# Optimization experiments

Measured on AMD Instinct MI355X. Metric: run time of the kernel, lower is better.

The kernel has to match this reference:

```python
import jax, jax.numpy as jnp
import numpy as np

N = 32767      # 2**15 - 1 nodes: complete binary tree, parent(i) = (i-1)//2
IN = 512       # in_channels
H = 256        # hidden_dim
OUT = 1        # output_dim
DEPTH = 15     # number of topological levels (static)


def setup_inputs() -> dict:
    key = jax.random.key(0)
    ks = jax.random.split(key, 8)
    x = jax.random.normal(ks[0], (N, IN), dtype=jnp.float32)
    # complete binary tree edge list: edge_index[0]=child, edge_index[1]=parent
    src = jnp.arange(1, N, dtype=jnp.int32)
    dst = (src - 1) // 2
    edge_index = jnp.stack([src, dst])  # [2, N-1]
    s = 1.0 / np.sqrt(H)  # torch LSTMCell/Linear default uniform init scale
    W_ih = jax.random.uniform(ks[1], (4 * H, IN), minval=-s, maxval=s, dtype=jnp.float32)
    W_hh = jax.random.uniform(ks[2], (4 * H, H), minval=-s, maxval=s, dtype=jnp.float32)
    b_ih = jax.random.uniform(ks[3], (4 * H,), minval=-s, maxval=s, dtype=jnp.float32)
    b_hh = jax.random.uniform(ks[4], (4 * H,), minval=-s, maxval=s, dtype=jnp.float32)
    W_fc = jax.random.uniform(ks[5], (OUT, H), minval=-s, maxval=s, dtype=jnp.float32)
    b_fc = jax.random.uniform(ks[6], (OUT,), minval=-s, maxval=s, dtype=jnp.float32)
    return {"x": x, "edge_index": edge_index, "W_ih": W_ih, "W_hh": W_hh,
            "b_ih": b_ih, "b_hh": b_hh, "W_fc": W_fc, "b_fc": b_fc}


def reference(x, edge_index, W_ih, W_hh, b_ih, b_hh, W_fc, b_fc):
    src, dst = edge_index[0], edge_index[1]
    # children count per parent (matches torch children_count loop)
    cnt = jax.ops.segment_sum(jnp.ones_like(src, dtype=x.dtype), dst, num_segments=N)
    cnt = jnp.maximum(cnt, 1.0)[:, None]  # [N,1]; leaves get zero child state anyway
    h = jnp.zeros((N, H), dtype=x.dtype)
    c = jnp.zeros((N, H), dtype=x.dtype)
    # topological sweep: deepest level first (children processed before parents)
    for d in range(DEPTH - 1, -1, -1):
        lo = 2 ** d - 1
        hi = min(2 ** (d + 1) - 1, N)  # level d node index range (static)
        # mean of already-computed child h/c states, gathered via edge list
        mean_h = jax.ops.segment_sum(h[src], dst, num_segments=N)[lo:hi] / cnt[lo:hi]
        mean_c = jax.ops.segment_sum(c[src], dst, num_segments=N)[lo:hi] / cnt[lo:hi]
        # torch LSTMCell: gates in (i, f, g, o) order
        gates = x[lo:hi] @ W_ih.T + b_ih + mean_h @ W_hh.T + b_hh  # [n_level, 4H]
        i, f, g, o = jnp.split(gates, 4, axis=-1)
        i, f, o = jax.nn.sigmoid(i), jax.nn.sigmoid(f), jax.nn.sigmoid(o)
        g = jnp.tanh(g)
        c_new = f * mean_c + i * g
        h_new = o * jnp.tanh(c_new)
        h = h.at[lo:hi].set(h_new)
        c = c.at[lo:hi].set(c_new)
    pooled = jnp.mean(h, axis=0, keepdims=True)  # [1, H]
    out = pooled @ W_fc.T + b_fc                 # [1, 1]
    return out.squeeze(-1)                       # [1]
```

## Files before the change

### kernel.cpp

```cpp
#include <hip/hip_runtime.h>
#include <hip/hip_cooperative_groups.h>
#include <math.h>

namespace cg = cooperative_groups;


#define N_NODES 32767
#define N_LEAF0 16383
#define IN_C    512
#define H_C     256

typedef __bf16 bf16x8 __attribute__((ext_vector_type(8)));
typedef float  f32x4  __attribute__((ext_vector_type(4)));

__device__ __forceinline__ void gload_lds16(const void* g, void* l) {
    __builtin_amdgcn_global_load_lds(
        (const __attribute__((address_space(1))) unsigned int*)g,
        (__attribute__((address_space(3))) unsigned int*)l,
        16, 0, 0);
}

__device__ __forceinline__ float fast_rcp(float x) { return __builtin_amdgcn_rcpf(x); }
__device__ __forceinline__ float sigm(float x)     { return fast_rcp(1.f + __expf(-x)); }
__device__ __forceinline__ float tanh_fast(float x){ return 2.f * fast_rcp(1.f + __expf(-2.f * x)) - 1.f; }

__global__ __launch_bounds__(256)
void conv_bf16_kernel(const float* __restrict__ src, __bf16* __restrict__ dst, int n8)
{
    const int i = blockIdx.x * 256 + threadIdx.x;
    if (i < n8) {
        const float4* s4 = (const float4*)src;
        const float4 a = s4[2 * i];
        const float4 b = s4[2 * i + 1];
        bf16x8 o;
        o[0] = (__bf16)a.x; o[1] = (__bf16)a.y; o[2] = (__bf16)a.z; o[3] = (__bf16)a.w;
        o[4] = (__bf16)b.x; o[5] = (__bf16)b.y; o[6] = (__bf16)b.z; o[7] = (__bf16)b.w;
        *(bf16x8*)(dst + 8 * i) = o;
    }
}

__global__ __launch_bounds__(256)
void bulk_xw(const float* __restrict__ x,
             const __bf16* __restrict__ wih,
             const float* __restrict__ b_ih,
             const float* __restrict__ b_hh,
             __bf16* __restrict__ hb,
             float* __restrict__ c,
             __bf16* __restrict__ gx)
{
    __shared__ __bf16 As[128 * 64];
    __shared__ __bf16 Bs[128 * 64];

    const int t    = threadIdx.x;
    const int lane = t & 63;
    const int wv   = t >> 6;
    const int wm   = wv >> 1;
    const int wn   = wv & 1;
    const int quad = lane >> 4;
    const int l15  = lane & 15;

    const int i  = blockIdx.x;
    const int cb = (i >> 3) & 7;
    const int mt = (i & 7) | ((i >> 6) << 3);
    const int m0 = mt * 128;

    f32x4 acc[4][4];
#pragma unroll
    for (int mi = 0; mi < 4; ++mi)
#pragma unroll
        for (int ni = 0; ni < 4; ++ni) acc[mi][ni] = (f32x4)0.f;

    for (int k0 = 0; k0 < IN_C; k0 += 64) {
#pragma unroll
        for (int e = 0; e < 4; ++e) {
            const int ch = (wv * 4 + e) * 64 + lane;
            const int nl = ch >> 3;
            const int k8 = (ch & 7) ^ (nl & 7);
            const int q  = (nl >> 4) & 3;
            const int cc = (nl & 15) | ((nl >> 6) << 4);
            const int grow = q * H_C + cb * 32 + cc;
            gload_lds16(wih + (size_t)grow * IN_C + k0 + k8 * 8,
                        (char*)Bs + (wv * 4 + e) * 1024);
        }
        {
            const int row  = t >> 1;
            const int kh   = (t & 1) * 32;
            const int node = min(m0 + row, N_NODES - 1);
            const float4* xs = (const float4*)(x + (size_t)node * IN_C + k0 + kh);
#pragma unroll
            for (int j = 0; j < 4; ++j) {
                const float4 v0 = xs[2 * j], v1 = xs[2 * j + 1];
                bf16x8 o;
                o[0] = (__bf16)v0.x; o[1] = (__bf16)v0.y; o[2] = (__bf16)v0.z; o[3] = (__bf16)v0.w;
                o[4] = (__bf16)v1.x; o[5] = (__bf16)v1.y; o[6] = (__bf16)v1.z; o[7] = (__bf16)v1.w;
                const int cs = ((kh >> 3) + j) ^ (row & 7);
                *(bf16x8*)(As + row * 64 + cs * 8) = o;
            }
        }
        __syncthreads();
#pragma unroll
        for (int ks = 0; ks < 2; ++ks) {
            bf16x8 af[4], bfr[4];
#pragma unroll
            for (int mi = 0; mi < 4; ++mi) {
                const int row = wm * 64 + mi * 16 + l15;
                af[mi] = *(const bf16x8*)(As + row * 64 + (((ks * 4 + quad) ^ (row & 7)) << 3));
            }
#pragma unroll
            for (int ni = 0; ni < 4; ++ni) {
                const int row = wn * 64 + ni * 16 + l15;
                bfr[ni] = *(const bf16x8*)(Bs + row * 64 + (((ks * 4 + quad) ^ (row & 7)) << 3));
            }
#pragma unroll
            for (int mi = 0; mi < 4; ++mi)
#pragma unroll
                for (int ni = 0; ni < 4; ++ni)
                    acc[mi][ni] = __builtin_amdgcn_mfma_f32_16x16x32_bf16(
                        af[mi], bfr[ni], acc[mi][ni], 0, 0, 0);
        }
        __syncthreads();
    }

    const int CH = cb * 32 + wn * 16 + l15;
    float bs[4];
#pragma unroll
    for (int q = 0; q < 4; ++q) bs[q] = b_ih[q * H_C + CH] + b_hh[q * H_C + CH];

#pragma unroll
    for (int mi = 0; mi < 4; ++mi) {
#pragma unroll
        for (int r = 0; r < 4; ++r) {
            const int m = m0 + wm * 64 + mi * 16 + quad * 4 + r;
            if (m >= N_NODES) continue;
            if (m >= N_LEAF0) {
                const float gi = sigm(acc[mi][0][r] + bs[0]);
                const float gf = sigm(acc[mi][1][r] + bs[1]);  (void)gf;
                const float gg = tanh_fast(acc[mi][2][r] + bs[2]);
                const float go = sigm(acc[mi][3][r] + bs[3]);
                const float cn = gi * gg;
                const float hn = go * tanh_fast(cn);
                c[(size_t)m * H_C + CH] = cn;
                hb[(size_t)m * H_C + CH] = (__bf16)hn;
            } else {
#pragma unroll
                for (int q = 0; q < 4; ++q)
                    gx[(size_t)m * 1024 + q * H_C + CH] = (__bf16)acc[mi][q][r];
            }
        }
    }
}

__global__ __launch_bounds__(256)
void level_hw(const __bf16* __restrict__ whh,
              const float* __restrict__ b_ih,
              const float* __restrict__ b_hh,
              const __bf16* __restrict__ gx,
              __bf16* __restrict__ hb,
              float* __restrict__ c,
              int lo, int n)
{
    __shared__ __bf16 As[128 * 32];
    __shared__ __bf16 Bs[128 * 32];

    const int t    = threadIdx.x;
    const int lane = t & 63;
    const int wv   = t >> 6;
    const int wm   = wv >> 1;
    const int wn   = wv & 1;
    const int quad = lane >> 4;
    const int l15  = lane & 15;

    const int i = blockIdx.x;
    int cb, mt;
    if (gridDim.x >= 64) { cb = (i >> 3) & 7; mt = (i & 7) | ((i >> 6) << 3); }
    else                 { cb = i & 7;        mt = i >> 3; }
    const int m0 = mt * 128;

    f32x4 acc[4][4];
#pragma unroll
    for (int mi = 0; mi < 4; ++mi)
#pragma unroll
        for (int ni = 0; ni < 4; ++ni) acc[mi][ni] = (f32x4)0.f;

    for (int k0 = 0; k0 < H_C; k0 += 32) {
#pragma unroll
        for (int e = 0; e < 2; ++e) {
            const int chunk = wv * 2 + e;
            const int nl    = chunk * 16 + (lane >> 2);
            const int q     = (nl >> 4) & 3;
            const int cc    = (nl & 15) + ((nl >> 6) << 4);
            const int grow  = q * H_C + cb * 32 + cc;
            const void* g = (const char*)(whh + grow * H_C + k0) + (lane & 3) * 16;
            gload_lds16(g, (char*)Bs + chunk * 1024);
        }
        {
            const int row  = t >> 1;
            const int kh   = (t & 1) * 16;
            const int node = lo + m0 + row;
            const int k2   = k0 + kh;
            const bf16x8* hl = (const bf16x8*)(hb + (size_t)(2 * node + 1) * H_C + k2);
            const bf16x8* hr = (const bf16x8*)(hb + (size_t)(2 * node + 2) * H_C + k2);
            const bf16x8 a0 = hl[0], a1 = hl[1], b0 = hr[0], b1 = hr[1];
            bf16x8 o0, o1;
#pragma unroll
            for (int j = 0; j < 8; ++j) {
                o0[j] = (__bf16)(0.5f * ((float)a0[j] + (float)b0[j]));
                o1[j] = (__bf16)(0.5f * ((float)a1[j] + (float)b1[j]));
            }
            bf16x8* dst = (bf16x8*)(As + row * 32 + kh);
            dst[0] = o0;
            dst[1] = o1;
        }
        __syncthreads();
        bf16x8 af[4], bfr[4];
#pragma unroll
        for (int mi = 0; mi < 4; ++mi)
            af[mi] = *(const bf16x8*)(As + (wm * 64 + mi * 16 + l15) * 32 + quad * 8);
#pragma unroll
        for (int ni = 0; ni < 4; ++ni)
            bfr[ni] = *(const bf16x8*)(Bs + (wn * 64 + ni * 16 + l15) * 32 + quad * 8);
#pragma unroll
        for (int mi = 0; mi < 4; ++mi)
#pragma unroll
            for (int ni = 0; ni < 4; ++ni)
                acc[mi][ni] = __builtin_amdgcn_mfma_f32_16x16x32_bf16(
                    af[mi], bfr[ni], acc[mi][ni], 0, 0, 0);
        __syncthreads();
    }

    const int CH = cb * 32 + wn * 16 + l15;
    float bs[4];
#pragma unroll
    for (int q = 0; q < 4; ++q) bs[q] = b_ih[q * H_C + CH] + b_hh[q * H_C + CH];

#pragma unroll
    for (int mi = 0; mi < 4; ++mi) {
#pragma unroll
        for (int r = 0; r < 4; ++r) {
            const int m = m0 + wm * 64 + mi * 16 + quad * 4 + r;
            if (m < n) {
                const int node = lo + m;
                const float g0 = acc[mi][0][r] + (float)gx[(size_t)node * 1024 + 0 * H_C + CH] + bs[0];
                const float g1 = acc[mi][1][r] + (float)gx[(size_t)node * 1024 + 1 * H_C + CH] + bs[1];
                const float g2 = acc[mi][2][r] + (float)gx[(size_t)node * 1024 + 2 * H_C + CH] + bs[2];
                const float g3 = acc[mi][3][r] + (float)gx[(size_t)node * 1024 + 3 * H_C + CH] + bs[3];
                const float gi = sigm(g0);
                const float gf = sigm(g1);
                const float gg = tanh_fast(g2);
                const float go = sigm(g3);
                const float mc = 0.5f * (c[(size_t)(2 * node + 1) * H_C + CH] +
                                         c[(size_t)(2 * node + 2) * H_C + CH]);
                const float cn = gf * mc + gi * gg;
                const float hn = go * tanh_fast(cn);
                c[(size_t)node * H_C + CH] = cn;
                hb[(size_t)node * H_C + CH] = (__bf16)hn;
            }
        }
    }
}

__global__ __launch_bounds__(256, 1)
void tail_levels(const __bf16* __restrict__ whh,
                 const float* __restrict__ b_ih,
                 const float* __restrict__ b_hh,
                 const __bf16* __restrict__ gx,
                 __bf16* __restrict__ hb,
                 const float* __restrict__ c)
{
    __shared__ __bf16 Ws[128][264];
    __shared__ __align__(16) char UAG[64 * 264 * 2];
    __shared__ float cl[2][64][33];

    const int t    = threadIdx.x;
    const int cb   = blockIdx.x;
    const int lane = t & 63;
    const int wq   = t >> 6;
    const int quad = lane >> 4;
    const int l15  = lane & 15;

    auto As = (__bf16(*)[264])UAG;
    auto Gs = (float(*)[64][33])UAG;

    {
        const int row = t >> 1;
        const int k0  = (t & 1) * 128;
        const int q   = row >> 5, cc = row & 31;
        const __bf16* src = whh + (size_t)(q * H_C + cb * 32 + cc) * H_C + k0;
#pragma unroll
        for (int j = 0; j < 16; ++j)
            *(bf16x8*)(&Ws[row][k0 + 8 * j]) = *(const bf16x8*)(src + 8 * j);
    }
    const int ecc = t & 31;
    const int erg = t >> 5;
    const int CH  = cb * 32 + ecc;
    float bsq[4];
#pragma unroll
    for (int q = 0; q < 4; ++q) bsq[q] = b_ih[q * H_C + CH] + b_hh[q * H_C + CH];

    cg::grid_group grid = cg::this_grid();

    for (int d = 6; d >= 0; --d) {
        const int n  = 1 << d;
        const int lo = n - 1;
        const int pp = d & 1;
        __syncthreads();
        {
            const int row  = t >> 2;
            const int kb   = (t & 3) * 64;
            const int node = lo + row;
            const bf16x8* hl = (const bf16x8*)(hb + (size_t)(2 * node + 1) * H_C + kb);
            const bf16x8* hr = (const bf16x8*)(hb + (size_t)(2 * node + 2) * H_C + kb);
#pragma unroll
            for (int j = 0; j < 8; ++j) {
                const bf16x8 a = hl[j], b = hr[j];
                bf16x8 o;
#pragma unroll
                for (int e = 0; e < 8; ++e)
                    o[e] = (__bf16)(0.5f * ((float)a[e] + (float)b[e]));
                *(bf16x8*)(&As[row][kb + 8 * j]) = o;
            }
        }
        __syncthreads();
        f32x4 acc[4][2];
#pragma unroll
        for (int mi = 0; mi < 4; ++mi)
#pragma unroll
            for (int ni = 0; ni < 2; ++ni) acc[mi][ni] = (f32x4)0.f;
        for (int kk = 0; kk < 8; ++kk) {
#pragma unroll
            for (int mi = 0; mi < 4; ++mi) {
                const bf16x8 af = *(const bf16x8*)(&As[mi * 16 + l15][kk * 32 + quad * 8]);
#pragma unroll
                for (int ni = 0; ni < 2; ++ni) {
                    const bf16x8 bf_ = *(const bf16x8*)(&Ws[wq * 32 + ni * 16 + l15][kk * 32 + quad * 8]);
                    acc[mi][ni] = __builtin_amdgcn_mfma_f32_16x16x32_bf16(af, bf_, acc[mi][ni], 0, 0, 0);
                }
            }
        }
        __syncthreads();
#pragma unroll
        for (int mi = 0; mi < 4; ++mi)
#pragma unroll
            for (int ni = 0; ni < 2; ++ni)
#pragma unroll
                for (int r = 0; r < 4; ++r)
                    Gs[wq][mi * 16 + quad * 4 + r][ni * 16 + l15] = acc[mi][ni][r];
        __syncthreads();
        for (int r = erg; r < n; r += 8) {
            const int node = lo + r;
            float g[4];
#pragma unroll
            for (int q = 0; q < 4; ++q)
                g[q] = Gs[q][r][ecc] + (float)gx[(size_t)node * 1024 + q * H_C + CH] + bsq[q];
            const float gi = sigm(g[0]);
            const float gf = sigm(g[1]);
            const float gg = tanh_fast(g[2]);
            const float go = sigm(g[3]);
            float mc;
            if (d == 6)
                mc = 0.5f * (c[(size_t)(2 * node + 1) * H_C + CH] +
                             c[(size_t)(2 * node + 2) * H_C + CH]);
            else
                mc = 0.5f * (cl[pp ^ 1][2 * r][ecc] + cl[pp ^ 1][2 * r + 1][ecc]);
            const float cn = gf * mc + gi * gg;
            const float hn = go * tanh_fast(cn);
            cl[pp][r][ecc] = cn;
            hb[(size_t)node * H_C + CH] = (__bf16)hn;
        }
        grid.sync();
    }
}

__global__ __launch_bounds__(256)
void reduce_rows(const __bf16* __restrict__ hb, float* __restrict__ part)
{
    __shared__ float sm[8][256];
    const int t  = threadIdx.x;
    const int b  = blockIdx.x;
    const int rg = t >> 5;
    const int c8 = (t & 31) * 8;
    float s[8];
#pragma unroll
    for (int j = 0; j < 8; ++j) s[j] = 0.f;
    for (int i2 = 0; i2 < 16; ++i2) {
        const int row = b * 128 + i2 * 8 + rg;
        if (row < N_NODES) {
            const bf16x8 v = *(const bf16x8*)(hb + (size_t)row * H_C + c8);
#pragma unroll
            for (int j = 0; j < 8; ++j) s[j] += (float)v[j];
        }
    }
#pragma unroll
    for (int j = 0; j < 8; ++j) sm[rg][c8 + j] = s[j];
    __syncthreads();
    float tot = 0.f;
#pragma unroll
    for (int g = 0; g < 8; ++g) tot += sm[g][t];
    part[b * H_C + t] = tot;
}

__global__ __launch_bounds__(256)
void reduce_final(const float* __restrict__ part,
                  const float* __restrict__ W_fc,
                  const float* __restrict__ b_fc,
                  float* __restrict__ out)
{
    __shared__ float sm[256];
    const int t = threadIdx.x;
    float s = 0.f;
    for (int j = 0; j < 256; ++j) s += part[j * H_C + t];
    s = s * (1.0f / (float)N_NODES) * W_fc[t];
    sm[t] = s;
    __syncthreads();
    for (int st = 128; st > 0; st >>= 1) {
        if (t < st) sm[t] += sm[t + st];
        __syncthreads();
    }
    if (t == 0) out[0] = sm[0] + b_fc[0];
}

extern "C" void kernel_launch(void* const* d_in, const int* in_sizes, int n_in,
                              void* d_out, int out_size, void* d_ws, size_t ws_size,
                              hipStream_t stream)
{
    const float* x    = (const float*)d_in[0];
    const float* W_ih = (const float*)d_in[2];
    const float* W_hh = (const float*)d_in[3];
    const float* b_ih = (const float*)d_in[4];
    const float* b_hh = (const float*)d_in[5];
    const float* W_fc = (const float*)d_in[6];
    const float* b_fc = (const float*)d_in[7];
    float* out = (float*)d_out;

    char* w = (char*)d_ws;
    __bf16* hb   = (__bf16*)w;  w += (size_t)N_NODES * H_C * 2;
    float*  c    = (float*)w;   w += (size_t)N_NODES * H_C * 4;
    __bf16* gx   = (__bf16*)w;  w += (size_t)N_LEAF0 * 1024 * 2;
    __bf16* wihb = (__bf16*)w;  w += (size_t)4 * H_C * IN_C * 2;
    __bf16* whhb = (__bf16*)w;  w += (size_t)4 * H_C * H_C * 2;
    float*  part = (float*)w;

    {
        const int n8i = (4 * H_C * IN_C) / 8;
        conv_bf16_kernel<<<(n8i + 255) / 256, 256, 0, stream>>>(W_ih, wihb, n8i);
        const int n8h = (4 * H_C * H_C) / 8;
        conv_bf16_kernel<<<(n8h + 255) / 256, 256, 0, stream>>>(W_hh, whhb, n8h);
    }

    bulk_xw<<<2048, 256, 0, stream>>>(x, wihb, b_ih, b_hh, hb, c, gx);

    for (int d = 13; d >= 7; --d) {
        const int n  = 1 << d;
        const int lo = n - 1;
        const int nm = (n + 127) / 128;
        level_hw<<<nm * 8, 256, 0, stream>>>(whhb, b_ih, b_hh, gx, hb, c, lo, n);
    }

    {
        const __bf16* a0 = whhb; const float* a1 = b_ih; const float* a2 = b_hh;
        const __bf16* a3 = gx;   __bf16* a4 = hb;        const float* a5 = c;
        void* targs[] = {&a0, &a1, &a2, &a3, &a4, &a5};
        hipError_t e = hipLaunchCooperativeKernel((const void*)tail_levels,
                                                  dim3(8), dim3(256), targs, 0, stream);
        if (e != hipSuccess) {
            for (int d = 6; d >= 0; --d) {
                const int n  = 1 << d;
                const int lo = n - 1;
                level_hw<<<8, 256, 0, stream>>>(whhb, b_ih, b_hh, gx, hb, c, lo, n);
            }
        }
    }

    reduce_rows<<<256, 256, 0, stream>>>(hb, part);
    reduce_final<<<1, 256, 0, stream>>>(part, W_fc, b_fc, out);
}
```

Before: 422.1 us.

## Fuse all tree levels and reduction into one cooperative kernel, pre-convert x to bf16

Converts x to bf16 in one combined conversion kernel and loads it into LDS with direct global-to-LDS loads in a new bulk GEMM. It interleaves the per-node gate pre-activations so they can be read and written as one vector. All levels from 13 down to 0, plus the mean-pool and FC reduction, now run inside a single 512-block cooperative kernel with grid syncs, which removes many kernel launches. The cost is that the small top levels use the generic tiled path on a wide grid instead of the specialised 8-block tail kernel, and the extra x copy adds memory traffic.

Measured after the change: 1.152 ms. 173% more time.

```diff
diff --git a/kernel.cpp b/kernel.cpp
--- a/kernel.cpp
+++ b/kernel.cpp
@@ -11,6 +11,7 @@
 #define H_C     256
 
 typedef __bf16 bf16x8 __attribute__((ext_vector_type(8)));
+typedef __bf16 bf16x4 __attribute__((ext_vector_type(4)));
 typedef float  f32x4  __attribute__((ext_vector_type(4)));
 
 __device__ __forceinline__ void gload_lds16(const void* g, void* l) {
@@ -25,28 +26,34 @@
 __device__ __forceinline__ float tanh_fast(float x){ return 2.f * fast_rcp(1.f + __expf(-2.f * x)) - 1.f; }
 
 __global__ __launch_bounds__(256)
-void conv_bf16_kernel(const float* __restrict__ src, __bf16* __restrict__ dst, int n8)
-{
-    const int i = blockIdx.x * 256 + threadIdx.x;
-    if (i < n8) {
-        const float4* s4 = (const float4*)src;
-        const float4 a = s4[2 * i];
-        const float4 b = s4[2 * i + 1];
+void conv3(const float* __restrict__ a, __bf16* __restrict__ da, int n8a,
+           const float* __restrict__ b, __bf16* __restrict__ db, int n8b,
+           const float* __restrict__ cx, __bf16* __restrict__ dc, int n8c)
+{
+    const int total = n8a + n8b + n8c;
+    for (int i = blockIdx.x * 256 + threadIdx.x; i < total; i += gridDim.x * 256) {
+        const float* s; __bf16* d; int j;
+        if (i < n8a)              { s = a;  d = da; j = i; }
+        else if (i < n8a + n8b)   { s = b;  d = db; j = i - n8a; }
+        else                      { s = cx; d = dc; j = i - n8a - n8b; }
+        const float4* s4 = (const float4*)s;
+        const float4 v0 = s4[2 * j];
+        const float4 v1 = s4[2 * j + 1];
         bf16x8 o;
-        o[0] = (__bf16)a.x; o[1] = (__bf16)a.y; o[2] = (__bf16)a.z; o[3] = (__bf16)a.w;
-        o[4] = (__bf16)b.x; o[5] = (__bf16)b.y; o[6] = (__bf16)b.z; o[7] = (__bf16)b.w;
-        *(bf16x8*)(dst + 8 * i) = o;
-    }
-}
-
-__global__ __launch_bounds__(256)
-void bulk_xw(const float* __restrict__ x,
-             const __bf16* __restrict__ wih,
-             const float* __restrict__ b_ih,
-             const float* __restrict__ b_hh,
-             __bf16* __restrict__ hb,
-             float* __restrict__ c,
-             __bf16* __restrict__ gx)
+        o[0] = (__bf16)v0.x; o[1] = (__bf16)v0.y; o[2] = (__bf16)v0.z; o[3] = (__bf16)v0.w;
+        o[4] = (__bf16)v1.x; o[5] = (__bf16)v1.y; o[6] = (__bf16)v1.z; o[7] = (__bf16)v1.w;
+        *(bf16x8*)(d + 8 * j) = o;
+    }
+}
+
+__global__ __launch_bounds__(256)
+void bulk_xw2(const __bf16* __restrict__ xb,
+              const __bf16* __restrict__ wih,
+              const float* __restrict__ b_ih,
+              const float* __restrict__ b_hh,
+              __bf16* __restrict__ hb,
+              float* __restrict__ c,
+              __bf16* __restrict__ gx)
 {
     __shared__ __bf16 As[128 * 64];
     __shared__ __bf16 Bs[128 * 64];
@@ -81,6 +88,105 @@
             const int grow = q * H_C + cb * 32 + cc;
             gload_lds16(wih + (size_t)grow * IN_C + k0 + k8 * 8,
                         (char*)Bs + (wv * 4 + e) * 1024);
+            int node = m0 + nl; if (node > N_NODES - 1) node = N_NODES - 1;
+            gload_lds16(xb + (size_t)node * IN_C + k0 + k8 * 8,
+                        (char*)As + (wv * 4 + e) * 1024);
+        }
+        __syncthreads();
+#pragma unroll
+        for (int ks = 0; ks < 2; ++ks) {
+            bf16x8 af[4], bfr[4];
+#pragma unroll
+            for (int mi = 0; mi < 4; ++mi) {
+                const int row = wm * 64 + mi * 16 + l15;
+                af[mi] = *(const bf16x8*)(As + row * 64 + (((ks * 4 + quad) ^ (row & 7)) << 3));
+            }
+#pragma unroll
+            for (int ni = 0; ni < 4; ++ni) {
+                const int row = wn * 64 + ni * 16 + l15;
+                bfr[ni] = *(const bf16x8*)(Bs + row * 64 + (((ks * 4 + quad) ^ (row & 7)) << 3));
+            }
+#pragma unroll
+            for (int mi = 0; mi < 4; ++mi)
+#pragma unroll
+                for (int ni = 0; ni < 4; ++ni)
+                    acc[mi][ni] = __builtin_amdgcn_mfma_f32_16x16x32_bf16(
+                        af[mi], bfr[ni], acc[mi][ni], 0, 0, 0);
+        }
+        __syncthreads();
+    }
+
+    const int CH = cb * 32 + wn * 16 + l15;
+    float bs4[4];
+#pragma unroll
+    for (int q = 0; q < 4; ++q) bs4[q] = b_ih[q * H_C + CH] + b_hh[q * H_C + CH];
+
+#pragma unroll
+    for (int mi = 0; mi < 4; ++mi) {
+#pragma unroll
+        for (int r = 0; r < 4; ++r) {
+            const int m = m0 + wm * 64 + mi * 16 + quad * 4 + r;
+            if (m >= N_NODES) continue;
+            if (m >= N_LEAF0) {
+                const float gi = sigm(acc[mi][0][r] + bs4[0]);
+                const float gg = tanh_fast(acc[mi][2][r] + bs4[2]);
+                const float go = sigm(acc[mi][3][r] + bs4[3]);
+                const float cn = gi * gg;
+                const float hn = go * tanh_fast(cn);
+                c[(size_t)m * H_C + CH] = cn;
+                hb[(size_t)m * H_C + CH] = (__bf16)hn;
+            } else {
+                bf16x4 o;
+#pragma unroll
+                for (int q = 0; q < 4; ++q) o[q] = (__bf16)acc[mi][q][r];
+                *(bf16x4*)(gx + ((size_t)m * H_C + CH) * 4) = o;
+            }
+        }
+    }
+}
+
+__global__ __launch_bounds__(256)
+void bulk_xw(const float* __restrict__ x,
+             const __bf16* __restrict__ wih,
+             const float* __restrict__ b_ih,
+             const float* __restrict__ b_hh,
+             __bf16* __restrict__ hb,
+             float* __restrict__ c,
+             __bf16* __restrict__ gx)
+{
+    __shared__ __bf16 As[128 * 64];
+    __shared__ __bf16 Bs[128 * 64];
+
+    const int t    = threadIdx.x;
+    const int lane = t & 63;
+    const int wv   = t >> 6;
+    const int wm   = wv >> 1;
+    const int wn   = wv & 1;
+    const int quad = lane >> 4;
+    const int l15  = lane & 15;
+
+    const int i  = blockIdx.x;
+    const int cb = (i >> 3) & 7;
+    const int mt = (i & 7) | ((i >> 6) << 3);
+    const int m0 = mt * 128;
+
+    f32x4 acc[4][4];
+#pragma unroll
+    for (int mi = 0; mi < 4; ++mi)
+#pragma unroll
+        for (int ni = 0; ni < 4; ++ni) acc[mi][ni] = (f32x4)0.f;
+
+    for (int k0 = 0; k0 < IN_C; k0 += 64) {
+#pragma unroll
+        for (int e = 0; e < 4; ++e) {
+            const int ch = (wv * 4 + e) * 64 + lane;
+            const int nl = ch >> 3;
+            const int k8 = (ch & 7) ^ (nl & 7);
+            const int q  = (nl >> 4) & 3;
+            const int cc = (nl & 15) | ((nl >> 6) << 4);
+            const int grow = q * H_C + cb * 32 + cc;
+            gload_lds16(wih + (size_t)grow * IN_C + k0 + k8 * 8,
+                        (char*)Bs + (wv * 4 + e) * 1024);
         }
         {
             const int row  = t >> 1;
@@ -122,9 +228,9 @@
     }
 
     const int CH = cb * 32 + wn * 16 + l15;
-    float bs[4];
-#pragma unroll
-    for (int q = 0; q < 4; ++q) bs[q] = b_ih[q * H_C + CH] + b_hh[q * H_C + CH];
+    float bs4[4];
+#pragma unroll
+    for (int q = 0; q < 4; ++q) bs4[q] = b_ih[q * H_C + CH] + b_hh[q * H_C + CH];
 
 #pragma unroll
     for (int mi = 0; mi < 4; ++mi) {
@@ -133,18 +239,120 @@
             const int m = m0 + wm * 64 + mi * 16 + quad * 4 + r;
             if (m >= N_NODES) continue;
             if (m >= N_LEAF0) {
-                const float gi = sigm(acc[mi][0][r] + bs[0]);
-                const float gf = sigm(acc[mi][1][r] + bs[1]);  (void)gf;
-                const float gg = tanh_fast(acc[mi][2][r] + bs[2]);
-                const float go = sigm(acc[mi][3][r] + bs[3]);
+                const float gi = sigm(acc[mi][0][r] + bs4[0]);
+                const float gg = tanh_fast(acc[mi][2][r] + bs4[2]);
+                const float go = sigm(acc[mi][3][r] + bs4[3]);
                 const float cn = gi * gg;
                 const float hn = go * tanh_fast(cn);
                 c[(size_t)m * H_C + CH] = cn;
                 hb[(size_t)m * H_C + CH] = (__bf16)hn;
             } else {
-#pragma unroll
-                for (int q = 0; q < 4; ++q)
-                    gx[(size_t)m * 1024 + q * H_C + CH] = (__bf16)acc[mi][q][r];
+                bf16x4 o;
+#pragma unroll
+                for (int q = 0; q < 4; ++q) o[q] = (__bf16)acc[mi][q][r];
+                *(bf16x4*)(gx + ((size_t)m * H_C + CH) * 4) = o;
+            }
+        }
+    }
+}
+
+__device__ __forceinline__ void level_tile(
+    const __bf16* __restrict__ whh, const float* __restrict__ b_ih,
+    const float* __restrict__ b_hh, const __bf16* __restrict__ gx,
+    __bf16* __restrict__ hb, float* __restrict__ c,
+    __bf16* As, __bf16* Bs, int lo, int n, int cb, int m0)
+{
+    const int t    = threadIdx.x;
+    const int lane = t & 63;
+    const int wv   = t >> 6;
+    const int wm   = wv >> 1;
+    const int wn   = wv & 1;
+    const int quad = lane >> 4;
+    const int l15  = lane & 15;
+
+    f32x4 acc[4][4];
+#pragma unroll
+    for (int mi = 0; mi < 4; ++mi)
+#pragma unroll
+        for (int ni = 0; ni < 4; ++ni) acc[mi][ni] = (f32x4)0.f;
+
+    for (int k0 = 0; k0 < H_C; k0 += 64) {
+#pragma unroll
+        for (int e = 0; e < 4; ++e) {
+            const int ch = (wv * 4 + e) * 64 + lane;
+            const int nl = ch >> 3;
+            const int k8 = (ch & 7) ^ (nl & 7);
+            const int q  = (nl >> 4) & 3;
+            const int cc = (nl & 15) | ((nl >> 6) << 4);
+            const int grow = q * H_C + cb * 32 + cc;
+            gload_lds16(whh + (size_t)grow * H_C + k0 + k8 * 8,
+                        (char*)Bs + (wv * 4 + e) * 1024);
+        }
+        {
+            const int row  = t >> 1;
+            const int kh   = (t & 1) * 32;
+            const int node = lo + m0 + row;
+            const int k2   = k0 + kh;
+            const bf16x8* hl = (const bf16x8*)(hb + (size_t)(2 * node + 1) * H_C + k2);
+            const bf16x8* hr = (const bf16x8*)(hb + (size_t)(2 * node + 2) * H_C + k2);
+#pragma unroll
+            for (int j = 0; j < 4; ++j) {
+                const bf16x8 a = hl[j], b = hr[j];
+                bf16x8 o;
+#pragma unroll
+                for (int e2 = 0; e2 < 8; ++e2)
+                    o[e2] = (__bf16)(0.5f * ((float)a[e2] + (float)b[e2]));
+                const int cs = ((kh >> 3) + j) ^ (row & 7);
+                *(bf16x8*)(As + row * 64 + cs * 8) = o;
+            }
+        }
+        __syncthreads();
+#pragma unroll
+        for (int ks = 0; ks < 2; ++ks) {
+            bf16x8 af[4], bfr[4];
+#pragma unroll
+            for (int mi = 0; mi < 4; ++mi) {
+                const int row = wm * 64 + mi * 16 + l15;
+                af[mi] = *(const bf16x8*)(As + row * 64 + (((ks * 4 + quad) ^ (row & 7)) << 3));
+            }
+#pragma unroll
+            for (int ni = 0; ni < 4; ++ni) {
+                const int row = wn * 64 + ni * 16 + l15;
+                bfr[ni] = *(const bf16x8*)(Bs + row * 64 + (((ks * 4 + quad) ^ (row & 7)) << 3));
+            }
+#pragma unroll
+            for (int mi = 0; mi < 4; ++mi)
+#pragma unroll
+                for (int ni = 0; ni < 4; ++ni)
+                    acc[mi][ni] = __builtin_amdgcn_mfma_f32_16x16x32_bf16(
+                        af[mi], bfr[ni], acc[mi][ni], 0, 0, 0);
+        }
+        __syncthreads();
+    }
+
+    const int CH = cb * 32 + wn * 16 + l15;
+    float bs4[4];
+#pragma unroll
+    for (int q = 0; q < 4; ++q) bs4[q] = b_ih[q * H_C + CH] + b_hh[q * H_C + CH];
+
+#pragma unroll
+    for (int mi = 0; mi < 4; ++mi) {
+#pragma unroll
+        for (int r = 0; r < 4; ++r) {
+            const int m = m0 + wm * 64 + mi * 16 + quad * 4 + r;
+            if (m < n) {
+                const int node = lo + m;
+                const bf16x4 gv = *(const bf16x4*)(gx + ((size_t)node * H_C + CH) * 4);
+                const float gi = sigm(acc[mi][0][r] + (float)gv[0] + bs4[0]);
+                const float gf = sigm(acc[mi][1][r] + (float)gv[1] + bs4[1]);
+                const float gg = tanh_fast(acc[mi][2][r] + (float)gv[2] + bs4[2]);
+                const float go = sigm(acc[mi][3][r] + (float)gv[3] + bs4[3]);
+                const float mc = 0.5f * (c[(size_t)(2 * node + 1) * H_C + CH] +
+                                         c[(size_t)(2 * node + 2) * H_C + CH]);
+                const float cn = gf * mc + gi * gg;
+                const float hn = go * tanh_fast(cn);
+                c[(size_t)node * H_C + CH] = cn;
+                hb[(size_t)node * H_C + CH] = (__bf16)hn;
             }
         }
     }
@@ -159,215 +367,84 @@
               float* __restrict__ c,
               int lo, int n)
 {
-    __shared__ __bf16 As[128 * 32];
-    __shared__ __bf16 Bs[128 * 32];
-
-    const int t    = threadIdx.x;
-    const int lane = t & 63;
-    const int wv   = t >> 6;
-    const int wm   = wv >> 1;
-    const int wn   = wv & 1;
-    const int quad = lane >> 4;
-    const int l15  = lane & 15;
-
+    __shared__ __bf16 As[128 * 64];
+    __shared__ __bf16 Bs[128 * 64];
     const int i = blockIdx.x;
     int cb, mt;
     if (gridDim.x >= 64) { cb = (i >> 3) & 7; mt = (i & 7) | ((i >> 6) << 3); }
     else                 { cb = i & 7;        mt = i >> 3; }
-    const int m0 = mt * 128;
-
-    f32x4 acc[4][4];
-#pragma unroll
-    for (int mi = 0; mi < 4; ++mi)
-#pragma unroll
-        for (int ni = 0; ni < 4; ++ni) acc[mi][ni] = (f32x4)0.f;
-
-    for (int k0 = 0; k0 < H_C; k0 += 32) {
-#pragma unroll
-        for (int e = 0; e < 2; ++e) {
-            const int chunk = wv * 2 + e;
-            const int nl    = chunk * 16 + (lane >> 2);
-            const int q     = (nl >> 4) & 3;
-            const int cc    = (nl & 15) + ((nl >> 6) << 4);
-            const int grow  = q * H_C + cb * 32 + cc;
-            const void* g = (const char*)(whh + grow * H_C + k0) + (lane & 3) * 16;
-            gload_lds16(g, (char*)Bs + chunk * 1024);
-        }
-        {
-            const int row  = t >> 1;
-            const int kh   = (t & 1) * 16;
-            const int node = lo + m0 + row;
-            const int k2   = k0 + kh;
-            const bf16x8* hl = (const bf16x8*)(hb + (size_t)(2 * node + 1) * H_C + k2);
-            const bf16x8* hr = (const bf16x8*)(hb + (size_t)(2 * node + 2) * H_C + k2);
-            const bf16x8 a0 = hl[0], a1 = hl[1], b0 = hr[0], b1 = hr[1];
-            bf16x8 o0, o1;
-#pragma unroll
-            for (int j = 0; j < 8; ++j) {
-                o0[j] = (__bf16)(0.5f * ((float)a0[j] + (float)b0[j]));
-                o1[j] = (__bf16)(0.5f * ((float)a1[j] + (float)b1[j]));
-            }
-            bf16x8* dst = (bf16x8*)(As + row * 32 + kh);
-            dst[0] = o0;
-            dst[1] = o1;
-        }
-        __syncthreads();
-        bf16x8 af[4], bfr[4];
-#pragma unroll
-        for (int mi = 0; mi < 4; ++mi)
-            af[mi] = *(const bf16x8*)(As + (wm * 64 + mi * 16 + l15) * 32 + quad * 8);
-#pragma unroll
-        for (int ni = 0; ni < 4; ++ni)
-            bfr[ni] = *(const bf16x8*)(Bs + (wn * 64 + ni * 16 + l15) * 32 + quad * 8);
-#pragma unroll
-        for (int mi = 0; mi < 4; ++mi)
-#pragma unroll
-            for (int ni = 0; ni < 4; ++ni)
-                acc[mi][ni] = __builtin_amdgcn_mfma_f32_16x16x32_bf16(
-                    af[mi], bfr[ni], acc[mi][ni], 0, 0, 0);
-        __syncthreads();
-    }
-
-    const int CH = cb * 32 + wn * 16 + l15;
-    float bs[4];
-#pragma unroll
-    for (int q = 0; q < 4; ++q) bs[q] = b_ih[q * H_C + CH] + b_hh[q * H_C + CH];
-
-#pragma unroll
-    for (int mi = 0; mi < 4; ++mi) {
-#pragma unroll
-        for (int r = 0; r < 4; ++r) {
-            const int m = m0 + wm * 64 + mi * 16 + quad * 4 + r;
-            if (m < n) {
-                const int node = lo + m;
-                const float g0 = acc[mi][0][r] + (float)gx[(size_t)node * 1024 + 0 * H_C + CH] + bs[0];
-                const float g1 = acc[mi][1][r] + (float)gx[(size_t)node * 1024 + 1 * H_C + CH] + bs[1];
-                const float g2 = acc[mi][2][r] + (float)gx[(size_t)node * 1024 + 2 * H_C + CH] + bs[2];
-                const float g3 = acc[mi][3][r] + (float)gx[(size_t)node * 1024 + 3 * H_C + CH] + bs[3];
-                const float gi = sigm(g0);
-                const float gf = sigm(g1);
-                const float gg = tanh_fast(g2);
-                const float go = sigm(g3);
-                const float mc = 0.5f * (c[(size_t)(2 * node + 1) * H_C + CH] +
-                                         c[(size_t)(2 * node + 2) * H_C + CH]);
-                const float cn = gf * mc + gi * gg;
-                const float hn = go * tanh_fast(cn);
-                c[(size_t)node * H_C + CH] = cn;
-                hb[(size_t)node * H_C + CH] = (__bf16)hn;
-            }
-        }
-    }
-}
-
-__global__ __launch_bounds__(256, 1)
-void tail_levels(const __bf16* __restrict__ whh,
+    level_tile(whh, b_ih, b_hh, gx, hb, c, As, Bs, lo, n, cb, mt * 128);
+}
+
+__global__ __launch_bounds__(256)
+void levels_coop(const __bf16* __restrict__ whh,
                  const float* __restrict__ b_ih,
                  const float* __restrict__ b_hh,
                  const __bf16* __restrict__ gx,
                  __bf16* __restrict__ hb,
-                 const float* __restrict__ c)
-{
-    __shared__ __bf16 Ws[128][264];
-    __shared__ __align__(16) char UAG[64 * 264 * 2];
-    __shared__ float cl[2][64][33];
-
-    const int t    = threadIdx.x;
-    const int cb   = blockIdx.x;
-    const int lane = t & 63;
-    const int wq   = t >> 6;
-    const int quad = lane >> 4;
-    const int l15  = lane & 15;
-
-    auto As = (__bf16(*)[264])UAG;
-    auto Gs = (float(*)[64][33])UAG;
-
-    {
-        const int row = t >> 1;
-        const int k0  = (t & 1) * 128;
-        const int q   = row >> 5, cc = row & 31;
-        const __bf16* src = whh + (size_t)(q * H_C + cb * 32 + cc) * H_C + k0;
-#pragma unroll
-        for (int j = 0; j < 16; ++j)
-            *(bf16x8*)(&Ws[row][k0 + 8 * j]) = *(const bf16x8*)(src + 8 * j);
-    }
-    const int ecc = t & 31;
-    const int erg = t >> 5;
-    const int CH  = cb * 32 + ecc;
-    float bsq[4];
-#pragma unroll
-    for (int q = 0; q < 4; ++q) bsq[q] = b_ih[q * H_C + CH] + b_hh[q * H_C + CH];
+                 float* __restrict__ c,
+                 const float* __restrict__ W_fc,
+                 const float* __restrict__ b_fc,
+                 float* __restrict__ part,
+                 float* __restrict__ out)
+{
+    __shared__ __bf16 As[128 * 64];
+    __shared__ __bf16 Bs[128 * 64];
 
     cg::grid_group grid = cg::this_grid();
-
-    for (int d = 6; d >= 0; --d) {
-        const int n  = 1 << d;
-        const int lo = n - 1;
-        const int pp = d & 1;
-        __syncthreads();
-        {
-            const int row  = t >> 2;
-            const int kb   = (t & 3) * 64;
-            const int node = lo + row;
-            const bf16x8* hl = (const bf16x8*)(hb + (size_t)(2 * node + 1) * H_C + kb);
-            const bf16x8* hr = (const bf16x8*)(hb + (size_t)(2 * node + 2) * H_C + kb);
-#pragma unroll
-            for (int j = 0; j < 8; ++j) {
-                const bf16x8 a = hl[j], b = hr[j];
-                bf16x8 o;
-#pragma unroll
-                for (int e = 0; e < 8; ++e)
-                    o[e] = (__bf16)(0.5f * ((float)a[e] + (float)b[e]));
-                *(bf16x8*)(&As[row][kb + 8 * j]) = o;
-            }
-        }
-        __syncthreads();
-        f32x4 acc[4][2];
-#pragma unroll
-        for (int mi = 0; mi < 4; ++mi)
-#pragma unroll
-            for (int ni = 0; ni < 2; ++ni) acc[mi][ni] = (f32x4)0.f;
-        for (int kk = 0; kk < 8; ++kk) {
-#pragma unroll
-            for (int mi = 0; mi < 4; ++mi) {
-                const bf16x8 af = *(const bf16x8*)(&As[mi * 16 + l15][kk * 32 + quad * 8]);
-#pragma unroll
-                for (int ni = 0; ni < 2; ++ni) {
-                    const bf16x8 bf_ = *(const bf16x8*)(&Ws[wq * 32 + ni * 16 + l15][kk * 32 + quad * 8]);
-                    acc[mi][ni] = __builtin_amdgcn_mfma_f32_16x16x32_bf16(af, bf_, acc[mi][ni], 0, 0, 0);
-                }
-            }
-        }
-        __syncthreads();
-#pragma unroll
-        for (int mi = 0; mi < 4; ++mi)
-#pragma unroll
-            for (int ni = 0; ni < 2; ++ni)
-#pragma unroll
-                for (int r = 0; r < 4; ++r)
-                    Gs[wq][mi * 16 + quad * 4 + r][ni * 16 + l15] = acc[mi][ni][r];
-        __syncthreads();
-        for (int r = erg; r < n; r += 8) {
-            const int node = lo + r;
-            float g[4];
-#pragma unroll
-            for (int q = 0; q < 4; ++q)
-                g[q] = Gs[q][r][ecc] + (float)gx[(size_t)node * 1024 + q * H_C + CH] + bsq[q];
-            const float gi = sigm(g[0]);
-            const float gf = sigm(g[1]);
-            const float gg = tanh_fast(g[2]);
-            const float go = sigm(g[3]);
-            float mc;
-            if (d == 6)
-                mc = 0.5f * (c[(size_t)(2 * node + 1) * H_C + CH] +
-                             c[(size_t)(2 * node + 2) * H_C + CH]);
-            else
-                mc = 0.5f * (cl[pp ^ 1][2 * r][ecc] + cl[pp ^ 1][2 * r + 1][ecc]);
-            const float cn = gf * mc + gi * gg;
-            const float hn = go * tanh_fast(cn);
-            cl[pp][r][ecc] = cn;
-            hb[(size_t)node * H_C + CH] = (__bf16)hn;
+    const int t  = threadIdx.x;
+    const int ib = blockIdx.x;
+
+    for (int d = 13; d >= 0; --d) {
+        const int n    = 1 << d;
+        const int lo   = n - 1;
+        const int nblk = ((n + 127) / 128) * 8;
+        if (ib < nblk) {
+            int cb, mt;
+            if (nblk >= 64) { cb = (ib >> 3) & 7; mt = (ib & 7) | ((ib >> 6) << 3); }
+            else            { cb = ib & 7;        mt = ib >> 3; }
+            level_tile(whh, b_ih, b_hh, gx, hb, c, As, Bs, lo, n, cb, mt * 128);
         }
         grid.sync();
+    }
+
+    if (ib < 256) {
+        const int rg = t >> 5;
+        const int c8 = (t & 31) * 8;
+        float s[8];
+#pragma unroll
+        for (int j = 0; j < 8; ++j) s[j] = 0.f;
+        for (int i2 = 0; i2 < 16; ++i2) {
+            const int row = ib * 128 + i2 * 8 + rg;
+            if (row < N_NODES) {
+                const bf16x8 v = *(const bf16x8*)(hb + (size_t)row * H_C + c8);
+#pragma unroll
+                for (int j = 0; j < 8; ++j) s[j] += (float)v[j];
+            }
+        }
+        __shared__ float sm[8][256];
+#pragma unroll
+        for (int j = 0; j < 8; ++j) sm[rg][c8 + j] = s[j];
+        __syncthreads();
+        float tot = 0.f;
+#pragma unroll
+        for (int g = 0; g < 8; ++g) tot += sm[g][t];
+        part[ib * H_C + t] = tot;
+    }
+    grid.sync();
+
+    if (ib == 0) {
+        float s = 0.f;
+        for (int j = 0; j < 256; ++j) s += part[j * H_C + t];
+        s = s * (1.0f / (float)N_NODES) * W_fc[t];
+        __shared__ float fm[256];
+        fm[t] = s;
+        __syncthreads();
+        for (int st = 128; st > 0; st >>= 1) {
+            if (t < st) fm[t] += fm[t + st];
+            __syncthreads();
+        }
+        if (t == 0) out[0] = fm[0] + b_fc[0];
     }
 }
 
@@ -433,44 +510,46 @@
     float* out = (float*)d_out;
 
     char* w = (char*)d_ws;
-    __bf16* hb   = (__bf16*)w;  w += (size_t)N_NODES * H_C * 2;
-    float*  c    = (float*)w;   w += (size_t)N_NODES * H_C * 4;
-    __bf16* gx   = (__bf16*)w;  w += (size_t)N_LEAF0 * 1024 * 2;
-    __bf16* wihb = (__bf16*)w;  w += (size_t)4 * H_C * IN_C * 2;
-    __bf16* whhb = (__bf16*)w;  w += (size_t)4 * H_C * H_C * 2;
-    float*  part = (float*)w;
+    size_t used = 0;
+    __bf16* hb   = (__bf16*)(w + used); used += (size_t)N_NODES * H_C * 2;
+    float*  c    = (float*)(w + used);  used += (size_t)N_NODES * H_C * 4;
+    __bf16* gx   = (__bf16*)(w + used); used += (size_t)N_LEAF0 * H_C * 4 * 2;
+    __bf16* wihb = (__bf16*)(w + used); used += (size_t)4 * H_C * IN_C * 2;
+    __bf16* whhb = (__bf16*)(w + used); used += (size_t)4 * H_C * H_C * 2;
+    float*  part = (float*)(w + used);  used += (size_t)256 * H_C * 4;
+    __bf16* xb   = (__bf16*)(w + used);
+    const size_t need_xb = used + (size_t)N_NODES * IN_C * 2 + 1024;
+    const bool have_xb = (ws_size >= need_xb);
 
     {
         const int n8i = (4 * H_C * IN_C) / 8;
-        conv_bf16_kernel<<<(n8i + 255) / 256, 256, 0, stream>>>(W_ih, wihb, n8i);
         const int n8h = (4 * H_C * H_C) / 8;
-        conv_bf16_kernel<<<(n8h + 255) / 256, 256, 0, stream>>>(W_hh, whhb, n8h);
-    }
-
-    bulk_xw<<<2048, 256, 0, stream>>>(x, wihb, b_ih, b_hh, hb, c, gx);
-
-    for (int d = 13; d >= 7; --d) {
-        const int n  = 1 << d;
-        const int lo = n - 1;
-        const int nm = (n + 127) / 128;
-        level_hw<<<nm * 8, 256, 0, stream>>>(whhb, b_ih, b_hh, gx, hb, c, lo, n);
-    }
+        const int n8x = have_xb ? (N_NODES * IN_C) / 8 : 0;
+        conv3<<<2048, 256, 0, stream>>>(W_ih, wihb, n8i, W_hh, whhb, n8h, x, xb, n8x);
+    }
+
+    if (have_xb)
+        bulk_xw2<<<2048, 256, 0, stream>>>(xb, wihb, b_ih, b_hh, hb, c, gx);
+    else
+        bulk_xw<<<2048, 256, 0, stream>>>(x, wihb, b_ih, b_hh, hb, c, gx);
 
     {
         const __bf16* a0 = whhb; const float* a1 = b_ih; const float* a2 = b_hh;
-        const __bf16* a3 = gx;   __bf16* a4 = hb;        const float* a5 = c;
-        void* targs[] = {&a0, &a1, &a2, &a3, &a4, &a5};
-        hipError_t e = hipLaunchCooperativeKernel((const void*)tail_levels,
-                                                  dim3(8), dim3(256), targs, 0, stream);
+        const __bf16* a3 = gx;   __bf16* a4 = hb;        float* a5 = c;
+        const float* a6 = W_fc;  const float* a7 = b_fc; float* a8 = part;
+        float* a9 = out;
+        void* targs[] = {&a0, &a1, &a2, &a3, &a4, &a5, &a6, &a7, &a8, &a9};
+        hipError_t e = hipLaunchCooperativeKernel((const void*)levels_coop,
+                                                  dim3(512), dim3(256), targs, 0, stream);
         if (e != hipSuccess) {
-            for (int d = 6; d >= 0; --d) {
+            for (int d = 13; d >= 0; --d) {
                 const int n  = 1 << d;
                 const int lo = n - 1;
-                level_hw<<<8, 256, 0, stream>>>(whhb, b_ih, b_hh, gx, hb, c, lo, n);
-            }
-        }
-    }
-
-    reduce_rows<<<256, 256, 0, stream>>>(hb, part);
-    reduce_final<<<1, 256, 0, stream>>>(part, W_fc, b_fc, out);
-}
+                const int nm = (n + 127) / 128;
+                level_hw<<<nm * 8, 256, 0, stream>>>(whhb, b_ih, b_hh, gx, hb, c, lo, n);
+            }
+            reduce_rows<<<256, 256, 0, stream>>>(hb, part);
+            reduce_final<<<1, 256, 0, stream>>>(part, W_fc, b_fc, out);
+        }
+    }
+}
```
